# Kernel tuning notes

Measured on AMD Instinct MI355X. Metric: run time of the kernel, lower is better.

Reference implementation:

```python
import jax, jax.numpy as jnp
import numpy as np

NUM_EMB = 8192
EMB_DIM = 32
LATENT = 1024
COMMIT = 0.25
CB_COST = 1.0


def _l2norm(x, eps=1e-12):
    # matches torch F.normalize: x / max(||x||, eps)
    n = jnp.sqrt(jnp.sum(x * x, axis=-1, keepdims=True))
    return x / jnp.maximum(n, eps)


def setup_inputs() -> dict:
    key = jax.random.key(0)
    k = jax.random.split(key, 6)
    B = 32768
    s_in = 1.0 / np.sqrt(LATENT)
    s_out = 1.0 / np.sqrt(EMB_DIM)
    return {
        "z_e": jax.random.normal(k[0], (B, LATENT), jnp.float32),
        "in_w": jax.random.uniform(k[1], (EMB_DIM, LATENT), jnp.float32, -s_in, s_in),
        "in_b": jax.random.uniform(k[2], (EMB_DIM,), jnp.float32, -s_in, s_in),
        "out_w": jax.random.uniform(k[3], (LATENT, EMB_DIM), jnp.float32, -s_out, s_out),
        "out_b": jax.random.uniform(k[4], (LATENT,), jnp.float32, -s_out, s_out),
        "codebook": jax.random.normal(k[5], (NUM_EMB, EMB_DIM), jnp.float32),
    }


def reference(z_e, in_w, in_b, out_w, out_b, codebook):
    # in_proj: [B, LATENT] -> [B, EMB_DIM]
    ze = z_e @ in_w.T + in_b
    zn = _l2norm(ze)                      # [B, E]
    wn = _l2norm(codebook)                # [Z, E]
    # squared euclidean distance between normalized vectors
    dist = (jnp.sum(zn * zn, axis=1, keepdims=True)
            - 2.0 * (zn @ wn.T)
            + jnp.sum(wn * wn, axis=1))   # [B, Z]
    idx = jnp.argmin(dist, axis=1)        # [B]
    z_q = codebook[idx]                   # [B, E] (unnormalized codebook lookup)
    enc_loss = jnp.mean((ze - jax.lax.stop_gradient(z_q)) ** 2)
    cb_loss = jnp.mean((z_q - jax.lax.stop_gradient(ze)) ** 2)
    loss = CB_COST * cb_loss + COMMIT * enc_loss
    # straight-through estimator
    z_st = ze + jax.lax.stop_gradient(z_q - ze)
    out = z_st @ out_w.T + out_b          # [B, LATENT]
    return out, loss, enc_loss, cb_loss, idx, ze
```

## Files before the change

### kernel.cpp

```cpp
#include <hip/hip_runtime.h>
#include <hip/hip_bf16.h>

#define B_SZ    32768
#define LAT     1024
#define EMB     32
#define ZCB     8192
#define NSPL    8
#define CPS     (ZCB / NSPL)
#define RESC_CAP 32768
#define EPS_MARGIN 2e-4f

#define OFF_LOSS  ((size_t)B_SZ * LAT)
#define OFF_ENC   (OFF_LOSS + 1)
#define OFF_CB    (OFF_LOSS + 2)
#define OFF_IDX   (OFF_LOSS + 3)
#define OFF_ZE    (OFF_IDX + B_SZ)

#define WS_PZE    0
#define WS_PB1    0
#define WS_PB2    262144
#define WS_PL15   524288
#define WS_CAND   786432
#define WS_OTH    819200
#define WS_ZEA    2097152
#define WS_ZNPK   3145728
#define WS_WPK    4194304
#define WS_IDXT   4456448
#define WS_CNT    4489216
#define WS_LIST   4489217
#define WS_LPART  4521985

typedef float  f32x4  __attribute__((ext_vector_type(4)));
typedef short  short8 __attribute__((ext_vector_type(8)));

__device__ __forceinline__ unsigned short f2bf(float x) {
    unsigned u = __float_as_uint(x);
    u += 0x7FFF + ((u >> 16) & 1);
    return (unsigned short)(u >> 16);
}
__device__ __forceinline__ float bf2f(unsigned short h) {
    return __uint_as_float(((unsigned)h) << 16);
}

__global__ __launch_bounds__(256) void knorm(const float* __restrict__ cb,
                                             short* __restrict__ wpk) {
    int e = threadIdx.x;
    int r = threadIdx.y;
    int row = blockIdx.x * 8 + r;
    float v = cb[row * EMB + e];
    float s = v * v;
    #pragma unroll
    for (int m = 16; m >= 1; m >>= 1) s += __shfl_xor(s, m, 64);
    float n = fmaxf(sqrtf(s), 1e-12f);
    float w = v / n;
    unsigned short h = f2bf(w);
    unsigned short l = f2bf(w - bf2f(h));
    wpk[row * 64 + e]      = (short)h;
    wpk[row * 64 + 32 + e] = (short)l;
}

#define KZB 64
#define KZS 68
__global__ __launch_bounds__(256) void kze2(const float* __restrict__ z_e,
                                            const float* __restrict__ in_w,
                                            float* __restrict__ pze) {
    __shared__ float zs[64 * KZS];
    __shared__ float wt[KZB * 32];
    int tid = threadIdx.x;
    size_t row0 = (size_t)blockIdx.x * 64;
    int ks = blockIdx.y;
    int rs = tid >> 2;
    int eg = tid & 3;
    int E  = eg * 8;

    float acc[8];
    #pragma unroll
    for (int j = 0; j < 8; ++j) acc[j] = 0.f;

    for (int c = 0; c < 512 / KZB; ++c) {
        int kb = ks * 512 + c * KZB;
        __syncthreads();
        #pragma unroll
        for (int i = 0; i < 4; ++i) {
            int t = tid + i * 256;
            int r = t >> 4, c4 = t & 15;
            float4 v = *(const float4*)(z_e + (row0 + r) * LAT + kb + c4 * 4);
            *(float4*)&zs[r * KZS + c4 * 4] = v;
        }
        #pragma unroll
        for (int i = 0; i < 2; ++i) {
            int t = tid + i * 256;
            int e = t >> 4, k4 = t & 15;
            float4 v = *(const float4*)(in_w + (size_t)e * LAT + kb + k4 * 4);
            float vv[4] = {v.x, v.y, v.z, v.w};
            #pragma unroll
            for (int j = 0; j < 4; ++j) {
                int k = k4 * 4 + j;
                wt[k * 32 + (e ^ ((k & 7) << 2))] = vv[j];
            }
        }
        __syncthreads();
        #pragma unroll 4
        for (int kq = 0; kq < KZB / 4; ++kq) {
            int k0 = kq * 4;
            float4 za = *(const float4*)&zs[rs * KZS + k0];
            float zav[4] = {za.x, za.y, za.z, za.w};
            #pragma unroll
            for (int i = 0; i < 4; ++i) {
                int k = k0 + i;
                int sw = (k & 7) << 2;
                float4 w0 = *(const float4*)&wt[k * 32 + (E ^ sw)];
                float4 w1 = *(const float4*)&wt[k * 32 + ((E + 4) ^ sw)];
                float wa[8] = {w0.x, w0.y, w0.z, w0.w, w1.x, w1.y, w1.z, w1.w};
                #pragma unroll
                for (int j = 0; j < 8; ++j)
                    acc[j] = fmaf(zav[i], wa[j], acc[j]);
            }
        }
    }
    size_t rb = (size_t)ks * B_SZ + row0;
    float* p0 = pze + (rb + rs) * EMB + E;
    *(float4*)p0       = make_float4(acc[0], acc[1], acc[2], acc[3]);
    *(float4*)(p0 + 4) = make_float4(acc[4], acc[5], acc[6], acc[7]);
}

__global__ __launch_bounds__(256) void kprep(const float* __restrict__ pze,
                                             const float* __restrict__ in_b,
                                             float* __restrict__ ze_out,
                                             float* __restrict__ ze_a,
                                             short* __restrict__ znpk) {
    int tid = threadIdx.x;
    size_t row = (size_t)blockIdx.x * 64 + (tid >> 2);
    int eg = tid & 3;
    const float* p0 = pze + row * 32 + eg * 8;
    const float* p1 = p0 + (size_t)B_SZ * 32;
    float4 a0 = *(const float4*)p0, a1 = *(const float4*)(p0 + 4);
    float4 b0 = *(const float4*)p1, b1 = *(const float4*)(p1 + 4);
    float4 c0 = *(const float4*)(in_b + eg * 8), c1 = *(const float4*)(in_b + eg * 8 + 4);
    float v[8];
    v[0] = a0.x + b0.x + c0.x; v[1] = a0.y + b0.y + c0.y;
    v[2] = a0.z + b0.z + c0.z; v[3] = a0.w + b0.w + c0.w;
    v[4] = a1.x + b1.x + c1.x; v[5] = a1.y + b1.y + c1.y;
    v[6] = a1.z + b1.z + c1.z; v[7] = a1.w + b1.w + c1.w;
    float nn = 0.f;
    #pragma unroll
    for (int i = 0; i < 8; ++i) nn = fmaf(v[i], v[i], nn);
    nn += __shfl_xor(nn, 1, 64);
    nn += __shfl_xor(nn, 2, 64);
    float n = fmaxf(sqrtf(nn), 1e-12f);

    *(float4*)(ze_a + row * 32 + eg * 8)     = make_float4(v[0], v[1], v[2], v[3]);
    *(float4*)(ze_a + row * 32 + eg * 8 + 4) = make_float4(v[4], v[5], v[6], v[7]);
    #pragma unroll
    for (int i = 0; i < 8; ++i) ze_out[row * 32 + eg * 8 + i] = v[i];

    short8 hv, lv;
    #pragma unroll
    for (int i = 0; i < 8; ++i) {
        float x = v[i] / n;
        unsigned short h = f2bf(x);
        unsigned short l = f2bf(x - bf2f(h));
        hv[i] = (short)h; lv[i] = (short)l;
    }
    *(short8*)(znpk + row * 64 + eg * 8)      = hv;
    *(short8*)(znpk + row * 64 + 32 + eg * 8) = lv;
}

__global__ __launch_bounds__(256) void kdistM(const short* __restrict__ znpk,
                                              const short* __restrict__ wpk,
                                              float* __restrict__ pb1,
                                              float* __restrict__ pb2,
                                              int*   __restrict__ pl15) {
    __shared__ short wch[2][128 * 64];
    int tid = threadIdx.x;
    int wave = tid >> 6, l = tid & 63;
    int l15 = l & 15, g = l >> 4;
    size_t rowbase = (size_t)blockIdx.x * 256 + wave * 64;
    int s = blockIdx.y;

    short8 zh[4], zl[4];
    #pragma unroll
    for (int rt = 0; rt < 4; ++rt) {
        const short8* p = (const short8*)(znpk + (rowbase + rt * 16 + l15) * 64 + g * 8);
        zh[rt] = p[0];
        zl[rt] = p[4];
    }
    f32x4 zero4 = {0.f, 0.f, 0.f, 0.f};
    float bb1[16];
    #pragma unroll
    for (int i = 0; i < 16; ++i) bb1[i] = -1e30f;

    int sw = (l15 & 7) << 4;
    int bhoff = ((g * 16) ^ sw) >> 1;
    int bloff = ((64 + g * 16) ^ sw) >> 1;

    const short* wsrc = wpk + (size_t)s * CPS * 64;

    #pragma unroll
    for (int i = 0; i < 4; ++i) {
        int t = tid + i * 256;
        int code = t >> 3, slot = t & 7;
        short8 v = *(const short8*)(wsrc + (size_t)code * 64 + slot * 8);
        int doff = (slot * 16) ^ ((code & 7) << 4);
        *(short8*)&wch[0][code * 64 + (doff >> 1)] = v;
    }
    __syncthreads();

    for (int c = 0; c < 8; ++c) {
        if (c + 1 < 8) {
            const short* src = wsrc + (size_t)(c + 1) * 128 * 64;
            #pragma unroll
            for (int i = 0; i < 4; ++i) {
                int t = tid + i * 256;
                int code = t >> 3, slot = t & 7;
                short8 v = *(const short8*)(src + (size_t)code * 64 + slot * 8);
                int doff = (slot * 16) ^ ((code & 7) << 4);
                *(short8*)&wch[(c + 1) & 1][code * 64 + (doff >> 1)] = v;
            }
        }
        const short* W = &wch[c & 1][0];
        #pragma unroll
        for (int tt = 0; tt < 8; ++tt) {
            const short* rowp = W + (tt * 16 + l15) * 64;
            short8 bh = *(const short8*)(rowp + bhoff);
            short8 bl = *(const short8*)(rowp + bloff);
            #pragma unroll
            for (int rt = 0; rt < 4; ++rt) {
                f32x4 acc = __builtin_amdgcn_mfma_f32_16x16x32_bf16(zh[rt], bh, zero4, 0, 0, 0);
                acc = __builtin_amdgcn_mfma_f32_16x16x32_bf16(zl[rt], bh, acc, 0, 0, 0);
                acc = __builtin_amdgcn_mfma_f32_16x16x32_bf16(zh[rt], bl, acc, 0, 0, 0);
                #pragma unroll
                for (int r = 0; r < 4; ++r) {
                    int slot = rt * 4 + r;
                    bb1[slot] = fmaxf(bb1[slot], acc[r]);
                }
            }
        }
        __syncthreads();
    }
    #pragma unroll
    for (int slot = 0; slot < 16; ++slot) {
        float B1 = bb1[slot], B2 = -1e30f;
        int ID = l15;
        #pragma unroll
        for (int m = 1; m <= 8; m <<= 1) {
            float ob1 = __shfl_xor(B1, m, 64);
            float ob2 = __shfl_xor(B2, m, 64);
            int   oid = __shfl_xor(ID, m, 64);
            float mn = fminf(B1, ob1);
            B2 = fmaxf(fmaxf(B2, ob2), mn);
            bool take = (ob1 > B1) || (ob1 == B1 && oid < ID);
            B1 = take ? ob1 : B1;
            ID = take ? oid : ID;
        }
        if (l15 == 0) {
            size_t row = rowbase + (size_t)(slot >> 2) * 16 + g * 4 + (slot & 3);
            pb1[(size_t)s * B_SZ + row] = B1;
            pb2[(size_t)s * B_SZ + row] = B2;
            pl15[(size_t)s * B_SZ + row] = ID;
        }
    }
}

__global__ __launch_bounds__(256) void kmergeArg(const float* __restrict__ pb1,
                                                 const float* __restrict__ pb2,
                                                 const int* __restrict__ pl15,
                                                 int* __restrict__ cand,
                                                 float* __restrict__ oth,
                                                 int* __restrict__ cnt) {
    if (blockIdx.x == 0 && threadIdx.x == 0) *cnt = 0;
    int row = blockIdx.x * 256 + threadIdx.x;
    float best1 = pb1[row], best2 = pb2[row];
    int c = pl15[row], wsn = 0;
    #pragma unroll
    for (int s = 1; s < NSPL; ++s) {
        float b  = pb1[(size_t)s * B_SZ + row];
        float sb = pb2[(size_t)s * B_SZ + row];
        int   li = pl15[(size_t)s * B_SZ + row];
        float mn = fminf(best1, b);
        best2 = fmaxf(fmaxf(best2, sb), mn);
        if (b > best1) { best1 = b; c = li; wsn = s; }
    }
    cand[row] = wsn * 16 + c;
    oth[row] = best2;
}

__global__ __launch_bounds__(256) void krecover(const float* __restrict__ ze_a,
                                                const float* __restrict__ cb,
                                                const int* __restrict__ cand,
                                                const float* __restrict__ oth,
                                                int* __restrict__ idxt,
                                                int* __restrict__ cnt,
                                                int* __restrict__ list) {
    int tid = threadIdx.x;
    int l = tid & 63;
    int gl = l & 7;
    int gj = l >> 3;
    int row = (blockIdx.x * 256 + tid) >> 6;
    int c = cand[row];
    int s = c >> 4, lc = c & 15;
    float4 z = *(const float4*)(ze_a + (size_t)row * 32 + gl * 4);
    float zz = fmaf(z.x, z.x, fmaf(z.y, z.y, fmaf(z.z, z.z, z.w * z.w)));
    zz += __shfl_xor(zz, 1, 64);
    zz += __shfl_xor(zz, 2, 64);
    zz += __shfl_xor(zz, 4, 64);
    float zinv = 1.f / fmaxf(sqrtf(zz), 1e-12f);
    z.x *= zinv; z.y *= zinv; z.z *= zinv; z.w *= zinv;

    float best = -1e30f; int bi = 0;
    #pragma unroll
    for (int b = 0; b < CPS / 16 / 8; ++b) {
        int t = b * 8 + gj;
        int j = s * CPS + t * 16 + lc;
        float4 w = *(const float4*)(cb + (size_t)j * 32 + gl * 4);
        float w2 = fmaf(w.x, w.x, fmaf(w.y, w.y, fmaf(w.z, w.z, w.w * w.w)));
        float dt = fmaf(z.x, w.x, fmaf(z.y, w.y, fmaf(z.z, w.z, z.w * w.w)));
        w2 += __shfl_xor(w2, 1, 64); dt += __shfl_xor(dt, 1, 64);
        w2 += __shfl_xor(w2, 2, 64); dt += __shfl_xor(dt, 2, 64);
        w2 += __shfl_xor(w2, 4, 64); dt += __shfl_xor(dt, 4, 64);
        float inv = 1.f / fmaxf(sqrtf(w2), 1e-12f);
        float m = dt * inv - 0.5f * (w2 * inv * inv);
        if (m > best || (m == best && j < bi)) { best = m; bi = j; }
    }
    #pragma unroll
    for (int mk = 8; mk <= 32; mk <<= 1) {
        float ob = __shfl_xor(best, mk, 64);
        int   oi = __shfl_xor(bi, mk, 64);
        bool take = (ob > best) || (ob == best && oi < bi);
        best = take ? ob : best;
        bi   = take ? oi : bi;
    }
    if (l == 0) {
        idxt[row] = bi;
        if (best - (oth[row] - 0.5f) < EPS_MARGIN) {
            int p = atomicAdd(cnt, 1);
            if (p < RESC_CAP) list[p] = row;
        }
    }
}

__global__ __launch_bounds__(256) void krescore(const float* __restrict__ ze_a,
                                                const float* __restrict__ cb,
                                                int* __restrict__ idxt,
                                                const int* __restrict__ cnt,
                                                const int* __restrict__ list) {
    __shared__ float bvs[4];
    __shared__ int   bis[4];
    int tid = threadIdx.x;
    int wave = tid >> 6, l = tid & 63;
    int gl = l & 7;
    int gj = l >> 3;
    int n = *cnt; if (n > RESC_CAP) n = RESC_CAP;
    for (int ii = blockIdx.x; ii < n; ii += gridDim.x) {
        int row = list[ii];
        float4 z = *(const float4*)(ze_a + (size_t)row * 32 + gl * 4);
        float zz = fmaf(z.x, z.x, fmaf(z.y, z.y, fmaf(z.z, z.z, z.w * z.w)));
        zz += __shfl_xor(zz, 1, 64);
        zz += __shfl_xor(zz, 2, 64);
        zz += __shfl_xor(zz, 4, 64);
        float zinv = 1.f / fmaxf(sqrtf(zz), 1e-12f);
        z.x *= zinv; z.y *= zinv; z.z *= zinv; z.w *= zinv;

        float best = -1e30f; int bi = 0;
        int jbase = wave * 2048 + gj;
        for (int b = 0; b < 32; ++b) {
            float w2v[8], dtv[8];
            #pragma unroll
            for (int cc = 0; cc < 8; ++cc) {
                int j = jbase + (b * 8 + cc) * 8;
                float4 w = *(const float4*)(cb + (size_t)j * 32 + gl * 4);
                w2v[cc] = fmaf(w.x, w.x, fmaf(w.y, w.y, fmaf(w.z, w.z, w.w * w.w)));
                dtv[cc] = fmaf(z.x, w.x, fmaf(z.y, w.y, fmaf(z.z, w.z, z.w * w.w)));
            }
            #pragma unroll
            for (int cc = 0; cc < 8; ++cc) {
                w2v[cc] += __shfl_xor(w2v[cc], 1, 64);
                dtv[cc] += __shfl_xor(dtv[cc], 1, 64);
            }
            #pragma unroll
            for (int cc = 0; cc < 8; ++cc) {
                w2v[cc] += __shfl_xor(w2v[cc], 2, 64);
                dtv[cc] += __shfl_xor(dtv[cc], 2, 64);
            }
            #pragma unroll
            for (int cc = 0; cc < 8; ++cc) {
                w2v[cc] += __shfl_xor(w2v[cc], 4, 64);
                dtv[cc] += __shfl_xor(dtv[cc], 4, 64);
            }
            #pragma unroll
            for (int cc = 0; cc < 8; ++cc) {
                int j = jbase + (b * 8 + cc) * 8;
                float inv = 1.f / fmaxf(sqrtf(w2v[cc]), 1e-12f);
                float m = dtv[cc] * inv - 0.5f * (w2v[cc] * inv * inv);
                if (m > best || (m == best && j < bi)) { best = m; bi = j; }
            }
        }
        #pragma unroll
        for (int mk = 8; mk <= 32; mk <<= 1) {
            float ob = __shfl_xor(best, mk, 64);
            int   oi = __shfl_xor(bi, mk, 64);
            bool take = (ob > best) || (ob == best && oi < bi);
            best = take ? ob : best;
            bi   = take ? oi : bi;
        }
        if (l == 0) { bvs[wave] = best; bis[wave] = bi; }
        __syncthreads();
        if (tid == 0) {
            float B = bvs[0]; int I = bis[0];
            #pragma unroll
            for (int w2i = 1; w2i < 4; ++w2i) {
                float ob = bvs[w2i]; int oi = bis[w2i];
                if (ob > B || (ob == B && oi < I)) { B = ob; I = oi; }
            }
            idxt[row] = I;
        }
        __syncthreads();
    }
}

__global__ __launch_bounds__(256) void kfinal(const int* __restrict__ idxt,
                                              const float* __restrict__ ze,
                                              const float* __restrict__ cb,
                                              float* __restrict__ out_idx,
                                              float* __restrict__ lpart) {
    int tid = threadIdx.x;
    int row = blockIdx.x * 256 + tid;
    int bidx = idxt[row];
    out_idx[row] = (float)bidx;

    const float4* zq4 = (const float4*)(cb + (size_t)bidx * EMB);
    const float4* ze4 = (const float4*)(ze + (size_t)row * EMB);
    float sq = 0.f;
    #pragma unroll
    for (int i = 0; i < 8; ++i) {
        float4 q = zq4[i], z = ze4[i];
        float dx = z.x - q.x, dy = z.y - q.y, dz = z.z - q.z, dw = z.w - q.w;
        sq += (dx * dx + dy * dy) + (dz * dz + dw * dw);
    }
    #pragma unroll
    for (int m = 1; m <= 32; m <<= 1) sq += __shfl_xor(sq, m, 64);
    __shared__ float red[4];
    if ((tid & 63) == 0) red[tid >> 6] = sq;
    __syncthreads();
    if (tid == 0) lpart[blockIdx.x] = (red[0] + red[1]) + (red[2] + red[3]);
}

__global__ void kloss(const float* __restrict__ lpart, float* __restrict__ dout) {
    float v = lpart[threadIdx.x];
    #pragma unroll
    for (int m = 1; m <= 32; m <<= 1) v += __shfl_xor(v, m, 64);
    __shared__ float tmp[2];
    if ((threadIdx.x & 63) == 0) tmp[threadIdx.x >> 6] = v;
    __syncthreads();
    if (threadIdx.x == 0) {
        float enc = (tmp[0] + tmp[1]) / (float)(B_SZ * EMB);
        dout[OFF_LOSS] = 1.0f * enc + 0.25f * enc;
        dout[OFF_ENC]  = enc;
        dout[OFF_CB]   = enc;
    }
}

__global__ __launch_bounds__(256) void kout(const float* __restrict__ ze_a,
                                            const int* __restrict__ idxt,
                                            const float* __restrict__ cb,
                                            const float* __restrict__ out_w,
                                            const float* __restrict__ out_b,
                                            float* __restrict__ out) {
    __shared__ float zsh[128 * EMB];
    __shared__ int ish[128];
    int tid = threadIdx.x;
    int col = blockIdx.x * 512 + tid * 2;
    size_t row0 = (size_t)blockIdx.y * 128;
    if (tid < 128) ish[tid] = idxt[row0 + tid];
    __syncthreads();
    #pragma unroll
    for (int i = 0; i < 4; ++i) {
        int flat = i * 256 + tid;
        int r = flat >> 3, q = flat & 7;
        float4 zv = *(const float4*)(ze_a + (row0 + r) * EMB + q * 4);
        float4 qv = *(const float4*)(cb + (size_t)ish[r] * EMB + q * 4);
        float4 o;
        o.x = zv.x + (qv.x - zv.x); o.y = zv.y + (qv.y - zv.y);
        o.z = zv.z + (qv.z - zv.z); o.w = zv.w + (qv.w - zv.w);
        *(float4*)&zsh[r * EMB + q * 4] = o;
    }
    float wa[32], wb[32];
    {
        const float4* wa4 = (const float4*)(out_w + (size_t)col * EMB);
        const float4* wb4 = (const float4*)(out_w + (size_t)(col + 1) * EMB);
        #pragma unroll
        for (int i = 0; i < 8; ++i) {
            float4 a = wa4[i]; wa[4*i]=a.x; wa[4*i+1]=a.y; wa[4*i+2]=a.z; wa[4*i+3]=a.w;
            float4 b = wb4[i]; wb[4*i]=b.x; wb[4*i+1]=b.y; wb[4*i+2]=b.z; wb[4*i+3]=b.w;
        }
    }
    float b0 = out_b[col], b1 = out_b[col + 1];
    __syncthreads();
    for (int rr = 0; rr < 128; ++rr) {
        const float4* zr4 = (const float4*)(zsh + rr * EMB);
        float a0 = b0, a1 = b1;
        #pragma unroll
        for (int q = 0; q < 8; ++q) {
            float4 z = zr4[q];
            a0 = fmaf(z.x, wa[4*q],   a0); a1 = fmaf(z.x, wb[4*q],   a1);
            a0 = fmaf(z.y, wa[4*q+1], a0); a1 = fmaf(z.y, wb[4*q+1], a1);
            a0 = fmaf(z.z, wa[4*q+2], a0); a1 = fmaf(z.z, wb[4*q+2], a1);
            a0 = fmaf(z.w, wa[4*q+3], a0); a1 = fmaf(z.w, wb[4*q+3], a1);
        }
        float2 o; o.x = a0; o.y = a1;
        *(float2*)(out + (row0 + rr) * LAT + col) = o;
    }
}

extern "C" void kernel_launch(void* const* d_in, const int* in_sizes, int n_in,
                              void* d_out, int out_size, void* d_ws, size_t ws_size,
                              hipStream_t stream) {
    const float* z_e   = (const float*)d_in[0];
    const float* in_w  = (const float*)d_in[1];
    const float* in_b  = (const float*)d_in[2];
    const float* out_w = (const float*)d_in[3];
    const float* out_b = (const float*)d_in[4];
    const float* cb    = (const float*)d_in[5];

    float* out = (float*)d_out;
    float* ws  = (float*)d_ws;
    float* pze   = ws + WS_PZE;
    float* pb1   = ws + WS_PB1;
    float* pb2   = ws + WS_PB2;
    int*   pl15  = (int*)(ws + WS_PL15);
    int*   cand  = (int*)(ws + WS_CAND);
    float* oth   = ws + WS_OTH;
    float* ze_a  = ws + WS_ZEA;
    short* znpk  = (short*)(ws + WS_ZNPK);
    short* wpk   = (short*)(ws + WS_WPK);
    int*   idxt  = (int*)(ws + WS_IDXT);
    int*   cnt   = (int*)(ws + WS_CNT);
    int*   list  = (int*)(ws + WS_LIST);
    float* lpart = ws + WS_LPART;

    knorm    <<<dim3(ZCB / 8), dim3(32, 8), 0, stream>>>(cb, wpk);
    kze2     <<<dim3(B_SZ / 64, 2), 256, 0, stream>>>(z_e, in_w, pze);
    kprep    <<<dim3(B_SZ / 64), 256, 0, stream>>>(pze, in_b, out + OFF_ZE, ze_a, znpk);
    kdistM   <<<dim3(B_SZ / 256, NSPL), 256, 0, stream>>>(znpk, wpk, pb1, pb2, pl15);
    kmergeArg<<<dim3(B_SZ / 256), 256, 0, stream>>>(pb1, pb2, pl15, cand, oth, cnt);
    krecover <<<dim3(B_SZ / 4), 256, 0, stream>>>(ze_a, cb, cand, oth, idxt, cnt, list);
    krescore <<<dim3(512), 256, 0, stream>>>(ze_a, cb, idxt, cnt, list);
    kfinal   <<<dim3(B_SZ / 256), 256, 0, stream>>>(idxt, ze_a, cb, out + OFF_IDX, lpart);
    kloss    <<<1, 128, 0, stream>>>(lpart, out);
    kout     <<<dim3(2, B_SZ / 128), 256, 0, stream>>>(ze_a, idxt, cb, out_w, out_b, out);
}
```

Measured before the change: 260.1 us.

## Fuse in-proj with prep, merge into recover, and loss/idx into output kernel

The split-K in-projection and its reduction/normalize kernel become one kernel that handles 32 rows per block over the full K range, so the partial ze buffer round trip through memory is gone. The per-split argmin merge moves into krecover, and the index write plus loss partials move into the first column-block of kout, with kloss reading 256 partials. The counter reset moves into knorm. This cuts the launch count from ten to seven and removes several intermediate buffers. In exchange, the in-projection kernel has no K-split parallelism and each of its threads does more serial work.

```diff
diff --git a/kernel.cpp b/kernel.cpp
--- a/kernel.cpp
+++ b/kernel.cpp
@@ -16,12 +16,9 @@
 #define OFF_IDX   (OFF_LOSS + 3)
 #define OFF_ZE    (OFF_IDX + B_SZ)
 
-#define WS_PZE    0
 #define WS_PB1    0
 #define WS_PB2    262144
 #define WS_PL15   524288
-#define WS_CAND   786432
-#define WS_OTH    819200
 #define WS_ZEA    2097152
 #define WS_ZNPK   3145728
 #define WS_WPK    4194304
@@ -32,6 +29,7 @@
 
 typedef float  f32x4  __attribute__((ext_vector_type(4)));
 typedef short  short8 __attribute__((ext_vector_type(8)));
+typedef short  s4v    __attribute__((ext_vector_type(4)));
 
 __device__ __forceinline__ unsigned short f2bf(float x) {
     unsigned u = __float_as_uint(x);
@@ -43,7 +41,9 @@
 }
 
 __global__ __launch_bounds__(256) void knorm(const float* __restrict__ cb,
-                                             short* __restrict__ wpk) {
+                                             short* __restrict__ wpk,
+                                             int* __restrict__ cnt) {
+    if (blockIdx.x == 0 && threadIdx.x == 0 && threadIdx.y == 0) *cnt = 0;
     int e = threadIdx.x;
     int r = threadIdx.y;
     int row = blockIdx.x * 8 + r;
@@ -61,109 +61,99 @@
 
 #define KZB 64
 #define KZS 68
-__global__ __launch_bounds__(256) void kze2(const float* __restrict__ z_e,
+__global__ __launch_bounds__(256) void kzeF(const float* __restrict__ z_e,
                                             const float* __restrict__ in_w,
-                                            float* __restrict__ pze) {
-    __shared__ float zs[64 * KZS];
+                                            const float* __restrict__ in_b,
+                                            float* __restrict__ ze_out,
+                                            float* __restrict__ ze_a,
+                                            short* __restrict__ znpk) {
+    __shared__ float zs[32 * KZS];
     __shared__ float wt[KZB * 32];
     int tid = threadIdx.x;
-    size_t row0 = (size_t)blockIdx.x * 64;
-    int ks = blockIdx.y;
-    int rs = tid >> 2;
-    int eg = tid & 3;
-    int E  = eg * 8;
-
-    float acc[8];
-    #pragma unroll
-    for (int j = 0; j < 8; ++j) acc[j] = 0.f;
-
-    for (int c = 0; c < 512 / KZB; ++c) {
-        int kb = ks * 512 + c * KZB;
-        __syncthreads();
-        #pragma unroll
-        for (int i = 0; i < 4; ++i) {
-            int t = tid + i * 256;
-            int r = t >> 4, c4 = t & 15;
-            float4 v = *(const float4*)(z_e + (row0 + r) * LAT + kb + c4 * 4);
-            *(float4*)&zs[r * KZS + c4 * 4] = v;
-        }
-        #pragma unroll
-        for (int i = 0; i < 2; ++i) {
-            int t = tid + i * 256;
-            int e = t >> 4, k4 = t & 15;
-            float4 v = *(const float4*)(in_w + (size_t)e * LAT + kb + k4 * 4);
-            float vv[4] = {v.x, v.y, v.z, v.w};
-            #pragma unroll
-            for (int j = 0; j < 4; ++j) {
-                int k = k4 * 4 + j;
-                wt[k * 32 + (e ^ ((k & 7) << 2))] = vv[j];
-            }
-        }
-        __syncthreads();
-        #pragma unroll 4
-        for (int kq = 0; kq < KZB / 4; ++kq) {
-            int k0 = kq * 4;
-            float4 za = *(const float4*)&zs[rs * KZS + k0];
-            float zav[4] = {za.x, za.y, za.z, za.w};
-            #pragma unroll
-            for (int i = 0; i < 4; ++i) {
-                int k = k0 + i;
-                int sw = (k & 7) << 2;
-                float4 w0 = *(const float4*)&wt[k * 32 + (E ^ sw)];
-                float4 w1 = *(const float4*)&wt[k * 32 + ((E + 4) ^ sw)];
-                float wa[8] = {w0.x, w0.y, w0.z, w0.w, w1.x, w1.y, w1.z, w1.w};
-                #pragma unroll
-                for (int j = 0; j < 8; ++j)
-                    acc[j] = fmaf(zav[i], wa[j], acc[j]);
-            }
-        }
-    }
-    size_t rb = (size_t)ks * B_SZ + row0;
-    float* p0 = pze + (rb + rs) * EMB + E;
-    *(float4*)p0       = make_float4(acc[0], acc[1], acc[2], acc[3]);
-    *(float4*)(p0 + 4) = make_float4(acc[4], acc[5], acc[6], acc[7]);
-}
-
-__global__ __launch_bounds__(256) void kprep(const float* __restrict__ pze,
-                                             const float* __restrict__ in_b,
-                                             float* __restrict__ ze_out,
-                                             float* __restrict__ ze_a,
-                                             short* __restrict__ znpk) {
-    int tid = threadIdx.x;
-    size_t row = (size_t)blockIdx.x * 64 + (tid >> 2);
-    int eg = tid & 3;
-    const float* p0 = pze + row * 32 + eg * 8;
-    const float* p1 = p0 + (size_t)B_SZ * 32;
-    float4 a0 = *(const float4*)p0, a1 = *(const float4*)(p0 + 4);
-    float4 b0 = *(const float4*)p1, b1 = *(const float4*)(p1 + 4);
-    float4 c0 = *(const float4*)(in_b + eg * 8), c1 = *(const float4*)(in_b + eg * 8 + 4);
-    float v[8];
-    v[0] = a0.x + b0.x + c0.x; v[1] = a0.y + b0.y + c0.y;
-    v[2] = a0.z + b0.z + c0.z; v[3] = a0.w + b0.w + c0.w;
-    v[4] = a1.x + b1.x + c1.x; v[5] = a1.y + b1.y + c1.y;
-    v[6] = a1.z + b1.z + c1.z; v[7] = a1.w + b1.w + c1.w;
+    size_t row0 = (size_t)blockIdx.x * 32;
+    int rs = tid >> 3;
+    int eg = tid & 7;
+    int E  = eg * 4;
+
+    float acc0[4], acc1[4];
+    #pragma unroll
+    for (int j = 0; j < 4; ++j) { acc0[j] = 0.f; acc1[j] = 0.f; }
+
+#define ZCHUNKS(CLO, CHI, ACC)                                                  \
+    for (int c = (CLO); c < (CHI); ++c) {                                       \
+        int kb = c * KZB;                                                       \
+        __syncthreads();                                                        \
+        _Pragma("unroll")                                                       \
+        for (int i = 0; i < 2; ++i) {                                           \
+            int t = tid + i * 256;                                              \
+            int r = t >> 4, c4 = t & 15;                                        \
+            float4 v = *(const float4*)(z_e + (row0 + r) * LAT + kb + c4 * 4);  \
+            *(float4*)&zs[r * KZS + c4 * 4] = v;                                \
+        }                                                                       \
+        _Pragma("unroll")                                                       \
+        for (int i = 0; i < 2; ++i) {                                           \
+            int t = tid + i * 256;                                              \
+            int e = t >> 4, k4 = t & 15;                                        \
+            float4 v = *(const float4*)(in_w + (size_t)e * LAT + kb + k4 * 4);  \
+            float vv[4] = {v.x, v.y, v.z, v.w};                                 \
+            _Pragma("unroll")                                                   \
+            for (int j = 0; j < 4; ++j) {                                       \
+                int k = k4 * 4 + j;                                             \
+                wt[k * 32 + (e ^ ((k & 7) << 2))] = vv[j];                      \
+            }                                                                   \
+        }                                                                       \
+        __syncthreads();                                                        \
+        _Pragma("unroll 4")                                                     \
+        for (int kq = 0; kq < KZB / 4; ++kq) {                                  \
+            int k0 = kq * 4;                                                    \
+            float4 za = *(const float4*)&zs[rs * KZS + k0];                     \
+            float zav[4] = {za.x, za.y, za.z, za.w};                            \
+            _Pragma("unroll")                                                   \
+            for (int i = 0; i < 4; ++i) {                                       \
+                int k = k0 + i;                                                 \
+                int sw = (k & 7) << 2;                                          \
+                float4 w0 = *(const float4*)&wt[k * 32 + (E ^ sw)];             \
+                float wa[4] = {w0.x, w0.y, w0.z, w0.w};                         \
+                _Pragma("unroll")                                               \
+                for (int j = 0; j < 4; ++j)                                     \
+                    ACC[j] = fmaf(zav[i], wa[j], ACC[j]);                       \
+            }                                                                   \
+        }                                                                       \
+    }
+
+    ZCHUNKS(0, 8, acc0)
+    ZCHUNKS(8, 16, acc1)
+#undef ZCHUNKS
+
+    float4 b4 = *(const float4*)(in_b + E);
+    float bias[4] = {b4.x, b4.y, b4.z, b4.w};
+    float v[4];
+    #pragma unroll
+    for (int j = 0; j < 4; ++j) v[j] = (acc0[j] + acc1[j]) + bias[j];
     float nn = 0.f;
     #pragma unroll
-    for (int i = 0; i < 8; ++i) nn = fmaf(v[i], v[i], nn);
+    for (int j = 0; j < 4; ++j) nn = fmaf(v[j], v[j], nn);
     nn += __shfl_xor(nn, 1, 64);
     nn += __shfl_xor(nn, 2, 64);
+    nn += __shfl_xor(nn, 4, 64);
     float n = fmaxf(sqrtf(nn), 1e-12f);
 
-    *(float4*)(ze_a + row * 32 + eg * 8)     = make_float4(v[0], v[1], v[2], v[3]);
-    *(float4*)(ze_a + row * 32 + eg * 8 + 4) = make_float4(v[4], v[5], v[6], v[7]);
-    #pragma unroll
-    for (int i = 0; i < 8; ++i) ze_out[row * 32 + eg * 8 + i] = v[i];
-
-    short8 hv, lv;
-    #pragma unroll
-    for (int i = 0; i < 8; ++i) {
-        float x = v[i] / n;
+    size_t row = row0 + rs;
+    *(float4*)(ze_a + row * 32 + E) = make_float4(v[0], v[1], v[2], v[3]);
+    #pragma unroll
+    for (int j = 0; j < 4; ++j) ze_out[row * 32 + E + j] = v[j];
+
+    s4v hv, lv;
+    #pragma unroll
+    for (int j = 0; j < 4; ++j) {
+        float x = v[j] / n;
         unsigned short h = f2bf(x);
-        unsigned short l = f2bf(x - bf2f(h));
-        hv[i] = (short)h; lv[i] = (short)l;
-    }
-    *(short8*)(znpk + row * 64 + eg * 8)      = hv;
-    *(short8*)(znpk + row * 64 + 32 + eg * 8) = lv;
+        unsigned short lo = f2bf(x - bf2f(h));
+        hv[j] = (short)h;
+        lv[j] = (short)lo;
+    }
+    *(s4v*)(znpk + row * 64 + E)      = hv;
+    *(s4v*)(znpk + row * 64 + 32 + E) = lv;
 }
 
 __global__ __launch_bounds__(256) void kdistM(const short* __restrict__ znpk,
@@ -262,33 +252,11 @@
     }
 }
 
-__global__ __launch_bounds__(256) void kmergeArg(const float* __restrict__ pb1,
-                                                 const float* __restrict__ pb2,
-                                                 const int* __restrict__ pl15,
-                                                 int* __restrict__ cand,
-                                                 float* __restrict__ oth,
-                                                 int* __restrict__ cnt) {
-    if (blockIdx.x == 0 && threadIdx.x == 0) *cnt = 0;
-    int row = blockIdx.x * 256 + threadIdx.x;
-    float best1 = pb1[row], best2 = pb2[row];
-    int c = pl15[row], wsn = 0;
-    #pragma unroll
-    for (int s = 1; s < NSPL; ++s) {
-        float b  = pb1[(size_t)s * B_SZ + row];
-        float sb = pb2[(size_t)s * B_SZ + row];
-        int   li = pl15[(size_t)s * B_SZ + row];
-        float mn = fminf(best1, b);
-        best2 = fmaxf(fmaxf(best2, sb), mn);
-        if (b > best1) { best1 = b; c = li; wsn = s; }
-    }
-    cand[row] = wsn * 16 + c;
-    oth[row] = best2;
-}
-
 __global__ __launch_bounds__(256) void krecover(const float* __restrict__ ze_a,
                                                 const float* __restrict__ cb,
-                                                const int* __restrict__ cand,
-                                                const float* __restrict__ oth,
+                                                const float* __restrict__ pb1,
+                                                const float* __restrict__ pb2,
+                                                const int* __restrict__ pl15,
                                                 int* __restrict__ idxt,
                                                 int* __restrict__ cnt,
                                                 int* __restrict__ list) {
@@ -296,9 +264,21 @@
     int l = tid & 63;
     int gl = l & 7;
     int gj = l >> 3;
-    int row = (blockIdx.x * 256 + tid) >> 6;
-    int c = cand[row];
-    int s = c >> 4, lc = c & 15;
+    int row = blockIdx.x * 4 + (tid >> 6);
+
+    float best1 = pb1[row], othv = pb2[row];
+    int c = pl15[row], wsn = 0;
+    #pragma unroll
+    for (int s2 = 1; s2 < NSPL; ++s2) {
+        float b  = pb1[(size_t)s2 * B_SZ + row];
+        float sb = pb2[(size_t)s2 * B_SZ + row];
+        int   li = pl15[(size_t)s2 * B_SZ + row];
+        float mn = fminf(best1, b);
+        othv = fmaxf(fmaxf(othv, sb), mn);
+        if (b > best1) { best1 = b; c = li; wsn = s2; }
+    }
+    int s = wsn, lc = c;
+
     float4 z = *(const float4*)(ze_a + (size_t)row * 32 + gl * 4);
     float zz = fmaf(z.x, z.x, fmaf(z.y, z.y, fmaf(z.z, z.z, z.w * z.w)));
     zz += __shfl_xor(zz, 1, 64);
@@ -332,7 +312,7 @@
     }
     if (l == 0) {
         idxt[row] = bi;
-        if (best - (oth[row] - 0.5f) < EPS_MARGIN) {
+        if (best - (othv - 0.5f) < EPS_MARGIN) {
             int p = atomicAdd(cnt, 1);
             if (p < RESC_CAP) list[p] = row;
         }
@@ -418,71 +398,43 @@
     }
 }
 
-__global__ __launch_bounds__(256) void kfinal(const int* __restrict__ idxt,
-                                              const float* __restrict__ ze,
-                                              const float* __restrict__ cb,
-                                              float* __restrict__ out_idx,
-                                              float* __restrict__ lpart) {
-    int tid = threadIdx.x;
-    int row = blockIdx.x * 256 + tid;
-    int bidx = idxt[row];
-    out_idx[row] = (float)bidx;
-
-    const float4* zq4 = (const float4*)(cb + (size_t)bidx * EMB);
-    const float4* ze4 = (const float4*)(ze + (size_t)row * EMB);
-    float sq = 0.f;
-    #pragma unroll
-    for (int i = 0; i < 8; ++i) {
-        float4 q = zq4[i], z = ze4[i];
-        float dx = z.x - q.x, dy = z.y - q.y, dz = z.z - q.z, dw = z.w - q.w;
-        sq += (dx * dx + dy * dy) + (dz * dz + dw * dw);
-    }
-    #pragma unroll
-    for (int m = 1; m <= 32; m <<= 1) sq += __shfl_xor(sq, m, 64);
-    __shared__ float red[4];
-    if ((tid & 63) == 0) red[tid >> 6] = sq;
-    __syncthreads();
-    if (tid == 0) lpart[blockIdx.x] = (red[0] + red[1]) + (red[2] + red[3]);
-}
-
-__global__ void kloss(const float* __restrict__ lpart, float* __restrict__ dout) {
-    float v = lpart[threadIdx.x];
-    #pragma unroll
-    for (int m = 1; m <= 32; m <<= 1) v += __shfl_xor(v, m, 64);
-    __shared__ float tmp[2];
-    if ((threadIdx.x & 63) == 0) tmp[threadIdx.x >> 6] = v;
-    __syncthreads();
-    if (threadIdx.x == 0) {
-        float enc = (tmp[0] + tmp[1]) / (float)(B_SZ * EMB);
-        dout[OFF_LOSS] = 1.0f * enc + 0.25f * enc;
-        dout[OFF_ENC]  = enc;
-        dout[OFF_CB]   = enc;
-    }
-}
-
 __global__ __launch_bounds__(256) void kout(const float* __restrict__ ze_a,
                                             const int* __restrict__ idxt,
                                             const float* __restrict__ cb,
                                             const float* __restrict__ out_w,
                                             const float* __restrict__ out_b,
-                                            float* __restrict__ out) {
+                                            float* __restrict__ out,
+                                            float* __restrict__ out_idx,
+                                            float* __restrict__ lpart) {
     __shared__ float zsh[128 * EMB];
     __shared__ int ish[128];
+    __shared__ float red[4];
     int tid = threadIdx.x;
     int col = blockIdx.x * 512 + tid * 2;
     size_t row0 = (size_t)blockIdx.y * 128;
+    bool bx0 = (blockIdx.x == 0);
     if (tid < 128) ish[tid] = idxt[row0 + tid];
     __syncthreads();
+    float sq = 0.f;
     #pragma unroll
     for (int i = 0; i < 4; ++i) {
         int flat = i * 256 + tid;
         int r = flat >> 3, q = flat & 7;
         float4 zv = *(const float4*)(ze_a + (row0 + r) * EMB + q * 4);
         float4 qv = *(const float4*)(cb + (size_t)ish[r] * EMB + q * 4);
+        if (bx0) {
+            float dx = zv.x - qv.x, dy = zv.y - qv.y, dz = zv.z - qv.z, dw = zv.w - qv.w;
+            sq += (dx * dx + dy * dy) + (dz * dz + dw * dw);
+        }
         float4 o;
         o.x = zv.x + (qv.x - zv.x); o.y = zv.y + (qv.y - zv.y);
         o.z = zv.z + (qv.z - zv.z); o.w = zv.w + (qv.w - zv.w);
         *(float4*)&zsh[r * EMB + q * 4] = o;
+    }
+    if (bx0) {
+        #pragma unroll
+        for (int m = 1; m <= 32; m <<= 1) sq += __shfl_xor(sq, m, 64);
+        if ((tid & 63) == 0) red[tid >> 6] = sq;
     }
     float wa[32], wb[32];
     {
@@ -496,6 +448,10 @@
     }
     float b0 = out_b[col], b1 = out_b[col + 1];
     __syncthreads();
+    if (bx0) {
+        if (tid == 0) lpart[blockIdx.y] = (red[0] + red[1]) + (red[2] + red[3]);
+        if (tid < 128) out_idx[row0 + tid] = (float)ish[tid];
+    }
     for (int rr = 0; rr < 128; ++rr) {
         const float4* zr4 = (const float4*)(zsh + rr * EMB);
         float a0 = b0, a1 = b1;
@@ -512,6 +468,21 @@
     }
 }
 
+__global__ void kloss(const float* __restrict__ lpart, float* __restrict__ dout) {
+    float v = lpart[threadIdx.x];
+    #pragma unroll
+    for (int m = 1; m <= 32; m <<= 1) v += __shfl_xor(v, m, 64);
+    __shared__ float tmp[4];
+    if ((threadIdx.x & 63) == 0) tmp[threadIdx.x >> 6] = v;
+    __syncthreads();
+    if (threadIdx.x == 0) {
+        float enc = ((tmp[0] + tmp[1]) + (tmp[2] + tmp[3])) / (float)(B_SZ * EMB);
+        dout[OFF_LOSS] = 1.0f * enc + 0.25f * enc;
+        dout[OFF_ENC]  = enc;
+        dout[OFF_CB]   = enc;
+    }
+}
+
 extern "C" void kernel_launch(void* const* d_in, const int* in_sizes, int n_in,
                               void* d_out, int out_size, void* d_ws, size_t ws_size,
                               hipStream_t stream) {
@@ -524,12 +495,9 @@
 
     float* out = (float*)d_out;
     float* ws  = (float*)d_ws;
-    float* pze   = ws + WS_PZE;
     float* pb1   = ws + WS_PB1;
     float* pb2   = ws + WS_PB2;
     int*   pl15  = (int*)(ws + WS_PL15);
-    int*   cand  = (int*)(ws + WS_CAND);
-    float* oth   = ws + WS_OTH;
     float* ze_a  = ws + WS_ZEA;
     short* znpk  = (short*)(ws + WS_ZNPK);
     short* wpk   = (short*)(ws + WS_WPK);
@@ -538,14 +506,12 @@
     int*   list  = (int*)(ws + WS_LIST);
     float* lpart = ws + WS_LPART;
 
-    knorm    <<<dim3(ZCB / 8), dim3(32, 8), 0, stream>>>(cb, wpk);
-    kze2     <<<dim3(B_SZ / 64, 2), 256, 0, stream>>>(z_e, in_w, pze);
-    kprep    <<<dim3(B_SZ / 64), 256, 0, stream>>>(pze, in_b, out + OFF_ZE, ze_a, znpk);
-    kdistM   <<<dim3(B_SZ / 256, NSPL), 256, 0, stream>>>(znpk, wpk, pb1, pb2, pl15);
-    kmergeArg<<<dim3(B_SZ / 256), 256, 0, stream>>>(pb1, pb2, pl15, cand, oth, cnt);
-    krecover <<<dim3(B_SZ / 4), 256, 0, stream>>>(ze_a, cb, cand, oth, idxt, cnt, list);
-    krescore <<<dim3(512), 256, 0, stream>>>(ze_a, cb, idxt, cnt, list);
-    kfinal   <<<dim3(B_SZ / 256), 256, 0, stream>>>(idxt, ze_a, cb, out + OFF_IDX, lpart);
-    kloss    <<<1, 128, 0, stream>>>(lpart, out);
-    kout     <<<dim3(2, B_SZ / 128), 256, 0, stream>>>(ze_a, idxt, cb, out_w, out_b, out);
-}
+    knorm   <<<dim3(ZCB / 8), dim3(32, 8), 0, stream>>>(cb, wpk, cnt);
+    kzeF    <<<dim3(B_SZ / 32), 256, 0, stream>>>(z_e, in_w, in_b, out + OFF_ZE, ze_a, znpk);
+    kdistM  <<<dim3(B_SZ / 256, NSPL), 256, 0, stream>>>(znpk, wpk, pb1, pb2, pl15);
+    krecover<<<dim3(B_SZ / 4), 256, 0, stream>>>(ze_a, cb, pb1, pb2, pl15, idxt, cnt, list);
+    krescore<<<dim3(512), 256, 0, stream>>>(ze_a, cb, idxt, cnt, list);
+    kout    <<<dim3(2, B_SZ / 128), 256, 0, stream>>>(ze_a, idxt, cb, out_w, out_b, out,
+                                                      out + OFF_IDX, lpart);
+    kloss   <<<1, 256, 0, stream>>>(lpart, out);
+}
```

Result: slower. 271.1 us (+4.2%).
